# Performance work log

Hardware: AMD Instinct MI355X
Metric: run time of the kernel (lower is better)

## Reference

```python
import jax, jax.numpy as jnp
import numpy as np

NUM_EMBEDDINGS = 8192
EMBEDDING_DIM = 128


def setup_inputs() -> dict:
    key = jax.random.key(0)
    k1, k2 = jax.random.split(key)
    inputs = jax.random.normal(k1, (8, 32, 32, EMBEDDING_DIM), dtype=jnp.float32)
    embedding_weight = jax.random.normal(k2, (NUM_EMBEDDINGS, EMBEDDING_DIM), dtype=jnp.float32)
    return {"inputs": inputs, "embedding_weight": embedding_weight}


def reference(inputs, embedding_weight):
    # inputs: [B, H, W, C] channels-last; embedding_weight: [K, C]
    input_shape = inputs.shape
    flat_input = inputs.reshape(-1, EMBEDDING_DIM)  # [N, C]

    distances = (
        jnp.sum(flat_input ** 2, axis=1, keepdims=True)
        + jnp.sum(embedding_weight ** 2, axis=1)
        - 2.0 * flat_input @ embedding_weight.T
    )
    encoding_indices = jnp.argmin(distances, axis=1)  # [N]

    # one-hot encodings (returned by the original module)
    encodings = jax.nn.one_hot(encoding_indices, NUM_EMBEDDINGS, dtype=jnp.float32)  # [N, K]

    # quantized via direct gather (same math as one_hot @ weight, no big matmul)
    quantized = embedding_weight[encoding_indices].reshape(input_shape)  # [B,H,W,C]

    # straight-through estimator
    quantized = inputs + jax.lax.stop_gradient(quantized - inputs)

    quantized_nchw = jnp.transpose(quantized, (0, 3, 1, 2))  # [B,C,H,W]
    return quantized_nchw, encodings
```

## Files before the change

### kernel.cpp

```cpp
#include <hip/hip_runtime.h>

typedef _Float16 f16x4 __attribute__((ext_vector_type(4)));
typedef _Float16 f16x8 __attribute__((ext_vector_type(8)));
typedef float    f32x16 __attribute__((ext_vector_type(16)));
typedef float    f32x4v __attribute__((ext_vector_type(4)));

#define HN_OFF   0u
#define BEST_OFF 32768u
#define ERH_OFF  98304u
#define ERL_OFF  (98304u + 2097152u)
#define XRH_OFF  (98304u + 2u * 2097152u)
#define XRL_OFF  (98304u + 3u * 2097152u)

#define OUT_Q    0
#define OUT_ENC  1048576


__global__ __launch_bounds__(256) void k1_convert(const float* __restrict__ x,
                                                  const float* __restrict__ e,
                                                  char* __restrict__ wsb) {
    int bx = blockIdx.x, tid = threadIdx.x;
    bool is_e = bx < 1024;
    const float* src = is_e ? e : x;
    int sec = is_e ? bx : bx - 1024;
    size_t off = (size_t)sec * 1024 + tid * 4;
    float4 v = *(const float4*)(src + off);

    f16x4 hi, lo;
    hi[0] = (_Float16)v.x; hi[1] = (_Float16)v.y;
    hi[2] = (_Float16)v.z; hi[3] = (_Float16)v.w;
    lo[0] = (_Float16)((v.x - (float)hi[0]) * 2048.0f);
    lo[1] = (_Float16)((v.y - (float)hi[1]) * 2048.0f);
    lo[2] = (_Float16)((v.z - (float)hi[2]) * 2048.0f);
    lo[3] = (_Float16)((v.w - (float)hi[3]) * 2048.0f);

    if (is_e) {
        int code = (int)(off >> 7);
        int c = (tid & 31) * 4;
        int tile = code >> 6, w = code & 63;
        int s = c >> 4, half = (c >> 3) & 1;
        size_t dst = (size_t)tile * 8192 + s * 1024 + w * 16 + half * 8 + (c & 7);
        *(f16x4*)((_Float16*)(wsb + ERH_OFF) + dst) = hi;
        *(f16x4*)((_Float16*)(wsb + ERL_OFF) + dst) = lo;

        float ss = v.x * v.x + v.y * v.y + v.z * v.z + v.w * v.w;
        for (int o = 16; o > 0; o >>= 1) ss += __shfl_down(ss, o, 32);
        if ((tid & 31) == 0)
            ((float*)(wsb + HN_OFF))[code] = 0.5f * ss;
    } else {
        _Float16* ph = (_Float16*)(wsb + XRH_OFF);
        _Float16* pl = (_Float16*)(wsb + XRL_OFF);
        *(f16x4*)(ph + off) = hi;
        *(f16x4*)(pl + off) = lo;
        if (sec < 32)
            ((unsigned long long*)(wsb + BEST_OFF))[sec * 256 + tid] = 0ull;
    }
}

__global__ __launch_bounds__(256, 2) void k2_mfma(char* __restrict__ wsb,
                                                  float* __restrict__ out) {
    const _Float16* xrh = (const _Float16*)(wsb + XRH_OFF);
    const _Float16* xrl = (const _Float16*)(wsb + XRL_OFF);
    const _Float16* erh = (const _Float16*)(wsb + ERH_OFF);
    const _Float16* erl = (const _Float16*)(wsb + ERL_OFF);
    const float* hn = (const float*)(wsb + HN_OFF);
    unsigned long long* bestg = (unsigned long long*)(wsb + BEST_OFF);

    int tid = threadIdx.x;
    int lane = tid & 63, wave = tid >> 6;
    int col = lane & 31, half = lane >> 5;
    int m = blockIdx.x;
    int by = m & 7, bx = m >> 3;
    int r0 = bx * 128;
    int k0g = by * 1024;
    int row = r0 + wave * 32 + col;

    f16x8 ah[8], al[8];
    #pragma unroll
    for (int s = 0; s < 8; s++) {
        ah[s] = *(const f16x8*)(xrh + (size_t)row * 128 + s * 16 + half * 8);
        al[s] = *(const f16x8*)(xrl + (size_t)row * 128 + s * 16 + half * 8);
    }

    int lane_eo = col * 16 + half * 8;
    const _Float16* phz = erh + (size_t)(k0g >> 6) * 8192;
    const _Float16* plz = erl + (size_t)(k0g >> 6) * 8192;

    float best[16];
    int bidx[16];
    #pragma unroll
    for (int i = 0; i < 16; i++) { best[i] = -3.0e38f; bidx[i] = 0; }

    f32x4v z4 = {0.f, 0.f, 0.f, 0.f};
    f32x4v* dstf = (f32x4v*)(out + OUT_ENC) + (size_t)(by * 64 + bx) * 32768 + tid;

    for (int t = 0; t < 16; t++) {
        const _Float16* ph = phz + (size_t)t * 8192;
        const _Float16* pl = plz + (size_t)t * 8192;
        #pragma unroll
        for (int sub = 0; sub < 2; sub++) {
            f32x16 a0, a1, a2;
            #pragma unroll
            for (int i = 0; i < 16; i++) { a0[i] = 0.f; a1[i] = 0.f; a2[i] = 0.f; }
            const _Float16* phs = ph + sub * 512 + lane_eo;
            const _Float16* pls = pl + sub * 512 + lane_eo;
            #pragma unroll
            for (int s = 0; s < 8; s++) {
                f16x8 bh = *(const f16x8*)(phs + s * 1024);
                f16x8 bl = *(const f16x8*)(pls + s * 1024);
                a0 = __builtin_amdgcn_mfma_f32_32x32x16_f16(ah[s], bh, a0, 0, 0, 0);
                a1 = __builtin_amdgcn_mfma_f32_32x32x16_f16(ah[s], bl, a1, 0, 0, 0);
                a2 = __builtin_amdgcn_mfma_f32_32x32x16_f16(al[s], bh, a2, 0, 0, 0);
            }
            #pragma unroll
            for (int i = 0; i < 4; i++)
                dstf[(t * 2 + sub) * 1024 + i * 256] = z4;

            int code = k0g + t * 64 + sub * 32 + col;
            float hnv = hn[code];
            #pragma unroll
            for (int r = 0; r < 16; r++) {
                float sc = a0[r] + (a1[r] + a2[r]) * (1.0f / 2048.0f) - hnv;
                if (sc > best[r]) { best[r] = sc; bidx[r] = code; }
            }
        }
    }

    #pragma unroll
    for (int r = 0; r < 16; r++) {
        float s = best[r];
        int bi = bidx[r];
        #pragma unroll
        for (int mm = 1; mm < 32; mm <<= 1) {
            float qs = __shfl_xor(s, mm, 64);
            int qi = __shfl_xor(bi, mm, 64);
            if (qs > s || (qs == s && qi < bi)) { s = qs; bi = qi; }
        }
        if (col == 0) {
            int rl = (r & 3) + 8 * (r >> 2) + 4 * half;
            unsigned ub = __float_as_uint(s);
            ub = ((int)ub < 0) ? ~ub : (ub | 0x80000000u);
            unsigned long long p = ((unsigned long long)ub << 32) |
                                   (unsigned long long)(0xFFFFFFFFu - (unsigned)bi);
            atomicMax(&bestg[r0 + wave * 32 + rl], p);
        }
    }
}

__global__ __launch_bounds__(256) void k3_final(const char* __restrict__ wsb,
                                                const float* __restrict__ wgt,
                                                float* __restrict__ out) {
    int bid = blockIdx.x;
    int n = (bid & 31) * 256 + threadIdx.x;
    int q = bid >> 5;
    unsigned long long p = ((const unsigned long long*)(wsb + BEST_OFF))[n];
    int bi = (int)(0xFFFFFFFFu - (unsigned)(p & 0xFFFFFFFFull));

    if (q == 0)
        out[(size_t)OUT_ENC + (size_t)n * 8192 + bi] = 1.0f;

    int bq = n >> 10, hw = n & 1023;
    float* o = out + (size_t)bq * 131072 + hw + (size_t)q * 32 * 1024;
    const float4* wrow = (const float4*)(wgt + (size_t)bi * 128) + q * 8;
    #pragma unroll
    for (int c4 = 0; c4 < 8; c4++) {
        float4 v = wrow[c4];
        o[(c4 * 4 + 0) * 1024] = v.x;
        o[(c4 * 4 + 1) * 1024] = v.y;
        o[(c4 * 4 + 2) * 1024] = v.z;
        o[(c4 * 4 + 3) * 1024] = v.w;
    }
}

extern "C" void kernel_launch(void* const* d_in, const int* in_sizes, int n_in,
                              void* d_out, int out_size, void* d_ws, size_t ws_size,
                              hipStream_t stream) {
    const float* x = (const float*)d_in[0];
    const float* e = (const float*)d_in[1];
    float* out = (float*)d_out;
    char* ws = (char*)d_ws;

    k1_convert<<<2048, 256, 0, stream>>>(x, e, ws);
    k2_mfma<<<512, 256, 0, stream>>>(ws, out);
    k3_final<<<128, 256, 0, stream>>>(ws, e, out);
}
```

Before: 329.5 us.

## Stage codebook tiles in LDS via async loads, swap MFMA operands, dedicate zeroing wave

The codebook hi/lo tiles are now double-buffered in shared memory using global_load_lds, so the next tile streams in while the current one feeds the MFMAs. The operands are swapped so codes lie along MFMA rows and each lane keeps a single running argmin, which removes the 16-way cross-lane reduction. A fifth wave per block only zero-fills the one-hot output. The grid doubles, each block now handles 64 rows, and the codebook layout in k1 is changed to match. The cost is extra barriers per tile and heavier LDS use per block.

```diff
diff --git a/kernel.cpp b/kernel.cpp
--- a/kernel.cpp
+++ b/kernel.cpp
@@ -15,6 +15,12 @@
 #define OUT_Q    0
 #define OUT_ENC  1048576
 
+
+__device__ __forceinline__ void gll16(const void* g, void* l) {
+    __builtin_amdgcn_global_load_lds(
+        (const __attribute__((address_space(1))) unsigned int*)g,
+        (__attribute__((address_space(3))) unsigned int*)l, 16, 0, 0);
+}
 
 __global__ __launch_bounds__(256) void k1_convert(const float* __restrict__ x,
                                                   const float* __restrict__ e,
@@ -37,9 +43,10 @@
     if (is_e) {
         int code = (int)(off >> 7);
         int c = (tid & 31) * 4;
-        int tile = code >> 6, w = code & 63;
-        int s = c >> 4, half = (c >> 3) & 1;
-        size_t dst = (size_t)tile * 8192 + s * 1024 + w * 16 + half * 8 + (c & 7);
+        int T = code >> 6, cs = (code >> 5) & 1, colc = code & 31;
+        int s = c >> 4, hf = (c >> 3) & 1;
+        size_t dst = (size_t)T * 8192 + cs * 4096 + s * 512 + hf * 256
+                   + colc * 8 + (c & 7);
         *(f16x4*)((_Float16*)(wsb + ERH_OFF) + dst) = hi;
         *(f16x4*)((_Float16*)(wsb + ERL_OFF) + dst) = lo;
 
@@ -57,12 +64,13 @@
     }
 }
 
-__global__ __launch_bounds__(256, 2) void k2_mfma(char* __restrict__ wsb,
+__global__ __launch_bounds__(320, 3) void k2_mfma(char* __restrict__ wsb,
                                                   float* __restrict__ out) {
+    __shared__ _Float16 lds_e[2][2][8192];
+    __shared__ float    lds_hn[1024];
+
     const _Float16* xrh = (const _Float16*)(wsb + XRH_OFF);
     const _Float16* xrl = (const _Float16*)(wsb + XRL_OFF);
-    const _Float16* erh = (const _Float16*)(wsb + ERH_OFF);
-    const _Float16* erl = (const _Float16*)(wsb + ERL_OFF);
     const float* hn = (const float*)(wsb + HN_OFF);
     unsigned long long* bestg = (unsigned long long*)(wsb + BEST_OFF);
 
@@ -70,79 +78,96 @@
     int lane = tid & 63, wave = tid >> 6;
     int col = lane & 31, half = lane >> 5;
     int m = blockIdx.x;
-    int by = m & 7, bx = m >> 3;
-    int r0 = bx * 128;
+    int by = m & 7, g = m >> 3;
     int k0g = by * 1024;
-    int row = r0 + wave * 32 + col;
-
-    f16x8 ah[8], al[8];
+    int r0 = g * 64;
+
+    if (wave == 4) {
+        f32x4v z4 = {0.f, 0.f, 0.f, 0.f};
+        f32x4v* dst = (f32x4v*)(out + OUT_ENC) + (size_t)m * 16384 + lane;
+        #pragma unroll 4
+        for (int i = 0; i < 256; i++)
+            dst[i * 64] = z4;
+        return;
+    }
+
+    int rset = wave & 1, cs = wave >> 1;
+    int row = r0 + rset * 32 + col;
+
+    f16x8 xh[8], xl[8];
     #pragma unroll
     for (int s = 0; s < 8; s++) {
-        ah[s] = *(const f16x8*)(xrh + (size_t)row * 128 + s * 16 + half * 8);
-        al[s] = *(const f16x8*)(xrl + (size_t)row * 128 + s * 16 + half * 8);
-    }
-
-    int lane_eo = col * 16 + half * 8;
-    const _Float16* phz = erh + (size_t)(k0g >> 6) * 8192;
-    const _Float16* plz = erl + (size_t)(k0g >> 6) * 8192;
-
-    float best[16];
-    int bidx[16];
-    #pragma unroll
-    for (int i = 0; i < 16; i++) { best[i] = -3.0e38f; bidx[i] = 0; }
-
-    f32x4v z4 = {0.f, 0.f, 0.f, 0.f};
-    f32x4v* dstf = (f32x4v*)(out + OUT_ENC) + (size_t)(by * 64 + bx) * 32768 + tid;
-
+        xh[s] = *(const f16x8*)(xrh + (size_t)row * 128 + s * 16 + half * 8);
+        xl[s] = *(const f16x8*)(xrl + (size_t)row * 128 + s * 16 + half * 8);
+    }
+
+    *(float4*)(lds_hn + tid * 4) = *(const float4*)(hn + k0g + tid * 4);
+
+    const char* psrc = (const char*)wsb + (cs ? ERL_OFF : ERH_OFF);
+
+    {
+        const char* pb = psrc + (size_t)(by * 16) * 16384 + rset * 8192;
+        char* ld = (char*)&lds_e[0][cs][0] + rset * 8192;
+        #pragma unroll
+        for (int j = 0; j < 8; j++)
+            gll16(pb + j * 1024 + lane * 16, ld + j * 1024);
+    }
+    __syncthreads();
+
+    float best = -3.0e38f;
+    int bidx = 0;
+
+    int b = 0;
     for (int t = 0; t < 16; t++) {
-        const _Float16* ph = phz + (size_t)t * 8192;
-        const _Float16* pl = plz + (size_t)t * 8192;
-        #pragma unroll
-        for (int sub = 0; sub < 2; sub++) {
-            f32x16 a0, a1, a2;
+        if (t < 15) {
+            const char* pb = psrc + (size_t)(by * 16 + t + 1) * 16384 + rset * 8192;
+            char* ld = (char*)&lds_e[b ^ 1][cs][0] + rset * 8192;
             #pragma unroll
-            for (int i = 0; i < 16; i++) { a0[i] = 0.f; a1[i] = 0.f; a2[i] = 0.f; }
-            const _Float16* phs = ph + sub * 512 + lane_eo;
-            const _Float16* pls = pl + sub * 512 + lane_eo;
+            for (int j = 0; j < 8; j++)
+                gll16(pb + j * 1024 + lane * 16, ld + j * 1024);
+        }
+
+        const _Float16* Ah = &lds_e[b][0][cs * 4096 + lane * 8];
+        const _Float16* Al = &lds_e[b][1][cs * 4096 + lane * 8];
+        f32x16 a0, a1, a2;
+        #pragma unroll
+        for (int i = 0; i < 16; i++) { a0[i] = 0.f; a1[i] = 0.f; a2[i] = 0.f; }
+        #pragma unroll
+        for (int s = 0; s < 8; s++) {
+            f16x8 eh = *(const f16x8*)(Ah + s * 512);
+            f16x8 el = *(const f16x8*)(Al + s * 512);
+            a0 = __builtin_amdgcn_mfma_f32_32x32x16_f16(eh, xh[s], a0, 0, 0, 0);
+            a1 = __builtin_amdgcn_mfma_f32_32x32x16_f16(el, xh[s], a1, 0, 0, 0);
+            a2 = __builtin_amdgcn_mfma_f32_32x32x16_f16(eh, xl[s], a2, 0, 0, 0);
+        }
+        int cb = k0g + t * 64 + cs * 32 + 4 * half;
+        #pragma unroll
+        for (int gq = 0; gq < 4; gq++) {
+            float4 h4 = *(const float4*)(lds_hn + t * 64 + cs * 32 + gq * 8 + half * 4);
             #pragma unroll
-            for (int s = 0; s < 8; s++) {
-                f16x8 bh = *(const f16x8*)(phs + s * 1024);
-                f16x8 bl = *(const f16x8*)(pls + s * 1024);
-                a0 = __builtin_amdgcn_mfma_f32_32x32x16_f16(ah[s], bh, a0, 0, 0, 0);
-                a1 = __builtin_amdgcn_mfma_f32_32x32x16_f16(ah[s], bl, a1, 0, 0, 0);
-                a2 = __builtin_amdgcn_mfma_f32_32x32x16_f16(al[s], bh, a2, 0, 0, 0);
+            for (int j = 0; j < 4; j++) {
+                int r = gq * 4 + j;
+                float hv = (j == 0) ? h4.x : (j == 1) ? h4.y : (j == 2) ? h4.z : h4.w;
+                float sc = a0[r] + (a1[r] + a2[r]) * (1.0f / 2048.0f) - hv;
+                int cv = cb + gq * 8 + j;
+                if (sc > best) { best = sc; bidx = cv; }
             }
-            #pragma unroll
-            for (int i = 0; i < 4; i++)
-                dstf[(t * 2 + sub) * 1024 + i * 256] = z4;
-
-            int code = k0g + t * 64 + sub * 32 + col;
-            float hnv = hn[code];
-            #pragma unroll
-            for (int r = 0; r < 16; r++) {
-                float sc = a0[r] + (a1[r] + a2[r]) * (1.0f / 2048.0f) - hnv;
-                if (sc > best[r]) { best[r] = sc; bidx[r] = code; }
-            }
-        }
-    }
-
-    #pragma unroll
-    for (int r = 0; r < 16; r++) {
-        float s = best[r];
-        int bi = bidx[r];
-        #pragma unroll
-        for (int mm = 1; mm < 32; mm <<= 1) {
-            float qs = __shfl_xor(s, mm, 64);
-            int qi = __shfl_xor(bi, mm, 64);
-            if (qs > s || (qs == s && qi < bi)) { s = qs; bi = qi; }
-        }
-        if (col == 0) {
-            int rl = (r & 3) + 8 * (r >> 2) + 4 * half;
-            unsigned ub = __float_as_uint(s);
+        }
+
+        __syncthreads();
+        b ^= 1;
+    }
+
+    {
+        float qs = __shfl_xor(best, 32, 64);
+        int qi = __shfl_xor(bidx, 32, 64);
+        if (qs > best || (qs == best && qi < bidx)) { best = qs; bidx = qi; }
+        if (half == 0) {
+            unsigned ub = __float_as_uint(best);
             ub = ((int)ub < 0) ? ~ub : (ub | 0x80000000u);
             unsigned long long p = ((unsigned long long)ub << 32) |
-                                   (unsigned long long)(0xFFFFFFFFu - (unsigned)bi);
-            atomicMax(&bestg[r0 + wave * 32 + rl], p);
+                                   (unsigned long long)(0xFFFFFFFFu - (unsigned)bidx);
+            atomicMax(&bestg[row], p);
         }
     }
 }
@@ -181,6 +206,6 @@
     char* ws = (char*)d_ws;
 
     k1_convert<<<2048, 256, 0, stream>>>(x, e, ws);
-    k2_mfma<<<512, 256, 0, stream>>>(ws, out);
+    k2_mfma<<<1024, 320, 0, stream>>>(ws, out);
     k3_final<<<128, 256, 0, stream>>>(ws, e, out);
 }
```

After: 325.8 us. About the same (-1.1%).
